# Kernel tuning notes

Hardware: AMD Instinct MI355X
Metric: run time of the kernel (lower is better)

Reference implementation:

```python
import jax, jax.numpy as jnp
import numpy as np

B, E, K = 2048, 16, 4
D_SF, D_OF, D_PPF, D_PVF = 512, 512, 256, 256
D = D_SF + D_OF + D_PPF + D_PVF  # 1536 = moe_input_size
H = 1024
N_OBJ, N_PRED = 36, 132
EPS = float(np.finfo(np.float64).eps)  # matches np.finfo(float).eps in combine
NOISE_EPS = 1e-2


def setup_inputs() -> dict:
    key = jax.random.key(0)
    ks = jax.random.split(key, 12)
    r = lambda i, shape, scale=1.0: (jax.random.normal(ks[i], shape, jnp.float32) * scale)
    return {
        "sf": r(0, (B, D_SF)),
        "of": r(1, (B, D_OF)),
        "ppf": r(2, (B, D_PPF)),
        "pvf": r(3, (B, D_PVF)),
        "w_gate": r(4, (D, E), 0.02),
        "w_noise": r(5, (D, E), 0.02),
        "W1": r(6, (E, D, H), 1.0 / np.sqrt(D)),
        "b1": jnp.zeros((E, H), jnp.float32),
        "W2": r(7, (E, H, H), 1.0 / np.sqrt(H)),
        "b2": jnp.zeros((E, H), jnp.float32),
        "Ws": r(8, (E, H, N_OBJ), 1.0 / np.sqrt(H)),
        "bs": jnp.zeros((E, N_OBJ), jnp.float32),
        "Wo": r(9, (E, H, N_OBJ), 1.0 / np.sqrt(H)),
        "bo": jnp.zeros((E, N_OBJ), jnp.float32),
        "Wp": r(10, (E, H, N_PRED), 1.0 / np.sqrt(H)),
        "bp": jnp.zeros((E, N_PRED), jnp.float32),
        "noise": r(11, (B, E)),
    }


def _noisy_top_k_gates(x, w_gate, w_noise, noise):
    """Shazeer noisy top-k gating -> sparse [B, E] gate matrix."""
    clean_logits = x @ w_gate                                   # [B, E]
    noise_stddev = jax.nn.softplus(x @ w_noise) + NOISE_EPS      # [B, E]
    logits = clean_logits + noise * noise_stddev
    top_vals, top_idx = jax.lax.top_k(logits, K)                 # [B, K]
    top_gates = jax.nn.softmax(top_vals, axis=-1)                # renormalized over top-k
    gates = jnp.zeros_like(logits)
    gates = gates.at[jnp.arange(x.shape[0])[:, None], top_idx].set(top_gates)
    return gates


def _combine(log_scores, gates):
    """SparseDispatcher.combine_expert_output, dense-equivalent.
    log_scores: [E, B, C] per-expert log-probs; gates: [B, E].
    output[b] = log(sum_e gates[b,e] * exp(log_scores[e,b])), eps where all-zero.
    gates==0 exactly zeroes the non-routed experts (same as sparse index_add).
    """
    w = gates.T[:, :, None]                                      # [E, B, 1]
    combined = jnp.sum(jnp.exp(log_scores) * w, axis=0)          # [B, C]
    combined = jnp.where(combined == 0, EPS, combined)
    return jnp.log(combined)


def reference(sf, of, ppf, pvf, w_gate, w_noise,
              W1, b1, W2, b2, Ws, bs, Wo, bo, Wp, bp, noise):
    x = jnp.concatenate([sf, of, ppf, pvf], axis=-1)             # [B, D]
    gates = _noisy_top_k_gates(x, w_gate, w_noise, noise)        # [B, E]

    # All-expert dense evaluation (grouped GEMM): 3-layer relu MLP trunk.
    h1 = jax.nn.relu(jnp.einsum('bd,edh->ebh', x, W1) + b1[:, None, :])   # [E, B, H]
    h2 = jax.nn.relu(jnp.einsum('ebh,ehg->ebg', h1, W2) + b2[:, None, :])  # [E, B, H]

    s_log = jax.nn.log_softmax(jnp.einsum('ebh,ehc->ebc', h2, Ws) + bs[:, None, :], axis=-1)
    o_log = jax.nn.log_softmax(jnp.einsum('ebh,ehc->ebc', h2, Wo) + bo[:, None, :], axis=-1)
    p_log = jax.nn.log_softmax(jnp.einsum('ebh,ehc->ebc', h2, Wp) + bp[:, None, :], axis=-1)

    s_out = _combine(s_log, gates)   # [B, N_OBJ]
    o_out = _combine(o_log, gates)   # [B, N_OBJ]
    p_out = _combine(p_log, gates)   # [B, N_PRED]
    return s_out, o_out, p_out
```

## Files before the change

kernel.cpp:

```cpp
#include <hip/hip_runtime.h>
#include <hip/hip_bf16.h>
#include <cstdint>

typedef __attribute__((ext_vector_type(8))) short short8;
typedef __attribute__((ext_vector_type(4))) float f32x4;

constexpr int B_ = 2048, E_ = 16, D_ = 1536, H_ = 1024;
constexpr int NHEAD = 256;
constexpr int TOTROWS = B_ * 4;
constexpr int MAXTILES = 80;
constexpr float EPS_ = 2.220446049250313e-16f;

__device__ __forceinline__ void gload_lds16(const void* g, void* l) {
  __builtin_amdgcn_global_load_lds((const __attribute__((address_space(1))) void*)g,
                                   (__attribute__((address_space(3))) void*)l,
                                   16, 0, 0);
}

__global__ __launch_bounds__(64) void zero_small(int* __restrict__ p, int n) {
  if ((int)threadIdx.x < n) p[threadIdx.x] = 0;
}

__global__ __launch_bounds__(256) void gate_logits(
    const float* __restrict__ sf, const float* __restrict__ of_,
    const float* __restrict__ ppf, const float* __restrict__ pvf,
    const float* __restrict__ wg, const float* __restrict__ wn,
    float* __restrict__ logits_all)
{
  __shared__ float xs[8][D_];
  const int b0 = blockIdx.x * 8;
  const int t = threadIdx.x;
  for (int i = t; i < 8 * (D_ / 4); i += 256) {
    const int row = i / (D_ / 4);
    const int c4 = i % (D_ / 4);
    const int b = b0 + row;
    const int d = c4 * 4;
    float4 v;
    if (d < 512)       v = ((const float4*)(sf  + (size_t)b * 512))[c4];
    else if (d < 1024) v = ((const float4*)(of_ + (size_t)b * 512))[c4 - 128];
    else if (d < 1280) v = ((const float4*)(ppf + (size_t)b * 256))[c4 - 256];
    else               v = ((const float4*)(pvf + (size_t)b * 256))[c4 - 320];
    *(float4*)&xs[row][d] = v;
  }
  __syncthreads();
  const int tok = t >> 5, out = t & 31;
  const int col = out & 15;
  const float* __restrict__ w = (out < 16) ? wg : wn;
  float a0 = 0.f, a1 = 0.f, a2 = 0.f, a3 = 0.f;
#pragma unroll 4
  for (int d = 0; d < D_; d += 4) {
    a0 += xs[tok][d + 0] * w[(d + 0) * 16 + col];
    a1 += xs[tok][d + 1] * w[(d + 1) * 16 + col];
    a2 += xs[tok][d + 2] * w[(d + 2) * 16 + col];
    a3 += xs[tok][d + 3] * w[(d + 3) * 16 + col];
  }
  logits_all[(size_t)(b0 + tok) * 32 + out] = (a0 + a1) + (a2 + a3);
}

__global__ __launch_bounds__(256) void topk_kernel(
    const float* __restrict__ logits_all, const float* __restrict__ noise,
    int* __restrict__ topidx, float* __restrict__ topw, int* __restrict__ counts)
{
  __shared__ int hist[E_];
  const int t = threadIdx.x;
  if (t < E_) hist[t] = 0;
  __syncthreads();
  const int b = blockIdx.x * 256 + t;
  if (b < B_) {
    float lg[16];
#pragma unroll
    for (int i = 0; i < 16; ++i) {
      const float clean = logits_all[(size_t)b * 32 + i];
      const float z = logits_all[(size_t)b * 32 + 16 + i];
      const float sp = (z > 0.f) ? (z + log1pf(expf(-z))) : log1pf(expf(z));
      lg[i] = clean + noise[b * 16 + i] * (sp + 1e-2f);
    }
    float tv[4]; int ti[4];
    unsigned used = 0;
#pragma unroll
    for (int k = 0; k < 4; ++k) {
      float best = -INFINITY; int bi = 0;
#pragma unroll
      for (int i = 0; i < 16; ++i)
        if (!((used >> i) & 1u) && lg[i] > best) { best = lg[i]; bi = i; }
      used |= 1u << bi; tv[k] = best; ti[k] = bi;
    }
    float s = 0.f, ex[4];
#pragma unroll
    for (int k = 0; k < 4; ++k) { ex[k] = expf(tv[k] - tv[0]); s += ex[k]; }
#pragma unroll
    for (int k = 0; k < 4; ++k) {
      topw[b * 4 + k] = ex[k] / s; topidx[b * 4 + k] = ti[k];
      atomicAdd(&hist[ti[k]], 1);
    }
  }
  __syncthreads();
  if (t < E_) atomicAdd(&counts[t], hist[t]);
}

__global__ __launch_bounds__(64) void schedule_kernel(
    const int* __restrict__ counts, int* __restrict__ offsets, int* __restrict__ ntiles,
    int* __restrict__ tile_e, int* __restrict__ tile_rb, int* __restrict__ tile_len)
{
  if (threadIdx.x != 0) return;
  int off = 0, nt = 0;
  for (int e = 0; e < E_; ++e) {
    offsets[e] = off;
    int c = counts[e];
    if (c < 0) c = 0;
    if (c > TOTROWS) c = TOTROWS;
    for (int m0 = 0; m0 < c && nt < MAXTILES; m0 += 128) {
      tile_e[nt] = e; tile_rb[nt] = off + m0;
      tile_len[nt] = (c - m0 < 128) ? (c - m0) : 128;
      ++nt;
    }
    off += c;
  }
  offsets[E_] = off;
  *ntiles = nt;
}

__global__ __launch_bounds__(256) void build_rows(
    const int* __restrict__ topidx, const int* __restrict__ offsets,
    int* __restrict__ cursor, int* __restrict__ rowtok, int* __restrict__ slot)
{
  const int b = blockIdx.x * 256 + threadIdx.x;
  if (b >= B_) return;
#pragma unroll
  for (int k = 0; k < 4; ++k) {
    const int e = topidx[b * 4 + k];
    const int p = atomicAdd(&cursor[e], 1);
    int row = offsets[e] + p;
    if (row < 0) row = 0;
    if (row >= TOTROWS) row = TOTROWS - 1;
    rowtok[row] = b;
    slot[b * 4 + k] = row;
  }
}

__global__ __launch_bounds__(256) void gather_x(
    const float* __restrict__ sf, const float* __restrict__ of_,
    const float* __restrict__ ppf, const float* __restrict__ pvf,
    const int* __restrict__ rowtok, __hip_bfloat16* __restrict__ xp)
{
  const int row = blockIdx.x;
  int b = rowtok[row];
  if (b < 0) b = 0;
  if (b >= B_) b = B_ - 1;
  for (int d = threadIdx.x; d < D_; d += 256) {
    float v;
    if (d < 512)       v = sf[b * 512 + d];
    else if (d < 1024) v = of_[b * 512 + (d - 512)];
    else if (d < 1280) v = ppf[b * 256 + (d - 1024)];
    else               v = pvf[b * 256 + (d - 1280)];
    xp[(size_t)row * D_ + d] = __float2bfloat16(v);
  }
}

__global__ __launch_bounds__(256) void transpose_bf16(
    const float* __restrict__ src, __hip_bfloat16* __restrict__ dst, int K, int N)
{
  __shared__ float tile[32][33];
  const int e = blockIdx.z;
  const int n0 = blockIdx.x * 32, k0 = blockIdx.y * 32;
  const int tx = threadIdx.x, ty = threadIdx.y;
  const float* s = src + (size_t)e * K * N;
  __hip_bfloat16* d = dst + (size_t)e * N * K;
#pragma unroll
  for (int r = 0; r < 4; ++r) {
    const int k = k0 + ty + r * 8;
    tile[ty + r * 8][tx] = s[(size_t)k * N + n0 + tx];
  }
  __syncthreads();
#pragma unroll
  for (int r = 0; r < 4; ++r) {
    const int n = n0 + ty + r * 8;
    d[(size_t)n * K + k0 + tx] = __float2bfloat16(tile[tx][ty + r * 8]);
  }
}

__global__ __launch_bounds__(256) void head_transpose(
    const float* __restrict__ Wsp, const float* __restrict__ Wop,
    const float* __restrict__ Wpp, __hip_bfloat16* __restrict__ dst)
{
  __shared__ float tile[32][33];
  const int e = blockIdx.z;
  const int k0 = blockIdx.x * 32;
  const int n0 = blockIdx.y * 32;
  const int tx = threadIdx.x, ty = threadIdx.y;
#pragma unroll
  for (int r = 0; r < 4; ++r) {
    const int k = k0 + ty + r * 8;
    const int n = n0 + tx;
    float v;
    if (n < 36)       v = Wsp[((size_t)e * H_ + k) * 36 + n];
    else if (n < 72)  v = Wop[((size_t)e * H_ + k) * 36 + (n - 36)];
    else if (n < 204) v = Wpp[((size_t)e * H_ + k) * 132 + (n - 72)];
    else              v = 0.f;
    tile[ty + r * 8][tx] = v;
  }
  __syncthreads();
#pragma unroll
  for (int r = 0; r < 4; ++r) {
    const int n = n0 + ty + r * 8;
    dst[((size_t)e * NHEAD + n) * H_ + k0 + tx] = __float2bfloat16(tile[tx][ty + r * 8]);
  }
}

__global__ __launch_bounds__(256) void pack_hbias(
    const float* __restrict__ bs, const float* __restrict__ bo,
    const float* __restrict__ bp, float* __restrict__ hb)
{
  const int e = blockIdx.x, t = threadIdx.x;
  float v = 0.f;
  if (t < 36)       v = bs[e * 36 + t];
  else if (t < 72)  v = bo[e * 36 + (t - 36)];
  else if (t < 204) v = bp[e * 132 + (t - 72)];
  hb[e * NHEAD + t] = v;
}

template <int EPI>
__global__ __launch_bounds__(256) void gemm_sp(
    const int* __restrict__ ntiles, const int* __restrict__ tile_e,
    const int* __restrict__ tile_rb, const int* __restrict__ tile_len,
    const __hip_bfloat16* __restrict__ Ap, int ldA,
    const __hip_bfloat16* __restrict__ Bm, size_t strideB,
    const float* __restrict__ bias,
    void* __restrict__ Cout, int ldC, int K)
{
  __shared__ __align__(16) __hip_bfloat16 lA[128 * 64];
  __shared__ __align__(16) __hip_bfloat16 lB[128 * 64];
  const int ti = blockIdx.x;
  int nt = *ntiles;
  if (nt > MAXTILES) nt = MAXTILES;
  if (ti >= nt) return;
  const int e = tile_e[ti] & 15, rb = tile_rb[ti], L = tile_len[ti];
  const int bn = blockIdx.y;
  const int t = threadIdx.x;
  const int w = t >> 6, lane = t & 63;
  const int wm = w >> 1, wn = w & 1;
  const __hip_bfloat16* Be = Bm + (size_t)e * strideB + (size_t)(bn * 128) * K;
  const int rsub = lane >> 3;
  const int csub = (lane & 7) * 8;

  int arows[4];
#pragma unroll
  for (int j = 0; j < 4; ++j) {
    int rloc = j * 32 + w * 8 + rsub;
    int r = rb + (rloc < L ? rloc : L - 1);
    if (r < 0) r = 0;
    if (r >= TOTROWS) r = TOTROWS - 1;
    arows[j] = r;
  }

  f32x4 acc[4][4];
#pragma unroll
  for (int m = 0; m < 4; ++m)
#pragma unroll
    for (int n = 0; n < 4; ++n) acc[m][n] = (f32x4){0.f, 0.f, 0.f, 0.f};

  const int KT = K >> 6;
  const int arow = wm * 64 + (lane & 15);
  const int brow = wn * 64 + (lane & 15);
  const int khalf = (lane >> 4) * 8;

  for (int kt = 0; kt < KT; ++kt) {
    const int k0 = kt << 6;
    __syncthreads();
#pragma unroll
    for (int j = 0; j < 4; ++j) {
      const int r = j * 32 + w * 8 + rsub;
      gload_lds16(Ap + (size_t)arows[j] * ldA + (k0 + csub), &lA[j * 2048 + w * 512]);
      gload_lds16(Be + (size_t)r * K + (k0 + csub), &lB[j * 2048 + w * 512]);
    }
    asm volatile("s_waitcnt vmcnt(0)" ::: "memory");
    __syncthreads();
#pragma unroll
    for (int kk = 0; kk < 2; ++kk) {
      short8 af[4], bfr[4];
#pragma unroll
      for (int m = 0; m < 4; ++m)
        af[m] = *(const short8*)&lA[(arow + m * 16) * 64 + kk * 32 + khalf];
#pragma unroll
      for (int n = 0; n < 4; ++n)
        bfr[n] = *(const short8*)&lB[(brow + n * 16) * 64 + kk * 32 + khalf];
#pragma unroll
      for (int m = 0; m < 4; ++m)
#pragma unroll
        for (int n = 0; n < 4; ++n)
          acc[m][n] = __builtin_amdgcn_mfma_f32_16x16x32_bf16(af[m], bfr[n], acc[m][n], 0, 0, 0);
    }
  }

  const int rbase = (lane >> 4) * 4, cbase = lane & 15;
#pragma unroll
  for (int n = 0; n < 4; ++n) {
    const int gcol = bn * 128 + wn * 64 + n * 16 + cbase;
    const float bv = bias[(size_t)e * ldC + gcol];
#pragma unroll
    for (int m = 0; m < 4; ++m) {
      const int rloc0 = wm * 64 + m * 16 + rbase;
#pragma unroll
      for (int j = 0; j < 4; ++j) {
        const int rloc = rloc0 + j;
        if (rloc < L && rb + rloc < TOTROWS) {
          float v = acc[m][n][j] + bv;
          const size_t idx = (size_t)(rb + rloc) * ldC + gcol;
          if (EPI == 0) {
            ((__hip_bfloat16*)Cout)[idx] = __float2bfloat16(v > 0.f ? v : 0.f);
          } else {
            ((float*)Cout)[idx] = v;
          }
        }
      }
    }
  }
}

__global__ __launch_bounds__(256) void combine_kernel(
    const float* __restrict__ logits, const int* __restrict__ slot,
    const float* __restrict__ topw, float* __restrict__ out)
{
  __shared__ float rows[4][204];
  __shared__ float lse[4][3];
  __shared__ float wk[4];
  const int b = blockIdx.x, t = threadIdx.x;
  if (t < 4) wk[t] = topw[b * 4 + t];
#pragma unroll
  for (int k = 0; k < 4; ++k) {
    int row = slot[b * 4 + k];
    if (row < 0) row = 0;
    if (row >= TOTROWS) row = TOTROWS - 1;
    if (t < 204) rows[k][t] = logits[(size_t)row * NHEAD + t];
  }
  __syncthreads();
  const int wv = t >> 6, lane = t & 63;
  const int segbase[3] = {0, 36, 72};
  const int segcnt[3] = {36, 36, 132};
  for (int s = 0; s < 3; ++s) {
    float mx = -INFINITY;
    for (int c = lane; c < segcnt[s]; c += 64) mx = fmaxf(mx, rows[wv][segbase[s] + c]);
    for (int o = 32; o > 0; o >>= 1) mx = fmaxf(mx, __shfl_xor(mx, o));
    float sum = 0.f;
    for (int c = lane; c < segcnt[s]; c += 64) sum += expf(rows[wv][segbase[s] + c] - mx);
    for (int o = 32; o > 0; o >>= 1) sum += __shfl_xor(sum, o);
    if (lane == 0) lse[wv][s] = mx + logf(sum);
  }
  __syncthreads();
  if (t < 204) {
    const int seg = t < 36 ? 0 : (t < 72 ? 1 : 2);
    float acc = 0.f;
    for (int k = 0; k < 4; ++k) acc += wk[k] * expf(rows[k][t] - lse[k][seg]);
    if (acc == 0.f) acc = EPS_;
    const float r = logf(acc);
    if (t < 36)      out[b * 36 + t] = r;
    else if (t < 72) out[73728 + b * 36 + (t - 36)] = r;
    else             out[147456 + b * 132 + (t - 72)] = r;
  }
}

extern "C" void kernel_launch(void* const* d_in, const int* in_sizes, int n_in,
                              void* d_out, int out_size, void* d_ws, size_t ws_size,
                              hipStream_t stream)
{
  (void)in_sizes; (void)n_in; (void)out_size; (void)ws_size;
  const float* sf      = (const float*)d_in[0];
  const float* of_     = (const float*)d_in[1];
  const float* ppf     = (const float*)d_in[2];
  const float* pvf     = (const float*)d_in[3];
  const float* w_gate  = (const float*)d_in[4];
  const float* w_noise = (const float*)d_in[5];
  const float* W1      = (const float*)d_in[6];
  const float* b1      = (const float*)d_in[7];
  const float* W2      = (const float*)d_in[8];
  const float* b2      = (const float*)d_in[9];
  const float* Ws      = (const float*)d_in[10];
  const float* bs      = (const float*)d_in[11];
  const float* Wo      = (const float*)d_in[12];
  const float* bo      = (const float*)d_in[13];
  const float* Wp      = (const float*)d_in[14];
  const float* bp      = (const float*)d_in[15];
  const float* noise   = (const float*)d_in[16];

  char* ws = (char*)d_ws;
  size_t off = 0;
  auto take = [&](size_t bytes) -> void* {
    void* p = ws + off; off += (bytes + 255) & ~(size_t)255; return p;
  };
  __hip_bfloat16* W1T = (__hip_bfloat16*)take((size_t)E_ * H_ * D_ * 2);
  __hip_bfloat16* W2T = (__hip_bfloat16*)take((size_t)E_ * H_ * H_ * 2);
  __hip_bfloat16* WhT = (__hip_bfloat16*)take((size_t)E_ * NHEAD * H_ * 2);
  float* hbias        = (float*)take((size_t)E_ * NHEAD * 4);
  __hip_bfloat16* xp  = (__hip_bfloat16*)take((size_t)TOTROWS * D_ * 2);
  __hip_bfloat16* h1p = (__hip_bfloat16*)take((size_t)TOTROWS * H_ * 2);
  __hip_bfloat16* h2p = (__hip_bfloat16*)take((size_t)TOTROWS * H_ * 2);
  float* logitsp      = (float*)take((size_t)TOTROWS * NHEAD * 4);
  float* logits_all   = (float*)take((size_t)B_ * 32 * 4);
  int* counts         = (int*)take(64 * 4);
  int* cursor         = (int*)take(64 * 4);
  int* offsets        = (int*)take(64 * 4);
  int* ntiles         = (int*)take(64 * 4);
  int* tile_e         = (int*)take(MAXTILES * 4);
  int* tile_rb        = (int*)take(MAXTILES * 4);
  int* tile_len       = (int*)take(MAXTILES * 4);
  int* topidx         = (int*)take((size_t)B_ * 4 * 4);
  float* topw         = (float*)take((size_t)B_ * 4 * 4);
  int* rowtok         = (int*)take((size_t)TOTROWS * 4);
  int* slot           = (int*)take((size_t)B_ * 4 * 4);

  zero_small<<<1, 64, 0, stream>>>(counts, E_);
  zero_small<<<1, 64, 0, stream>>>(cursor, E_);
  gate_logits<<<B_ / 8, 256, 0, stream>>>(sf, of_, ppf, pvf, w_gate, w_noise, logits_all);
  topk_kernel<<<B_ / 256, 256, 0, stream>>>(logits_all, noise, topidx, topw, counts);
  schedule_kernel<<<1, 64, 0, stream>>>(counts, offsets, ntiles, tile_e, tile_rb, tile_len);
  build_rows<<<(B_ + 255) / 256, 256, 0, stream>>>(topidx, offsets, cursor, rowtok, slot);
  gather_x<<<TOTROWS, 256, 0, stream>>>(sf, of_, ppf, pvf, rowtok, xp);

  transpose_bf16<<<dim3(H_ / 32, D_ / 32, E_), dim3(32, 8), 0, stream>>>(W1, W1T, D_, H_);
  transpose_bf16<<<dim3(H_ / 32, H_ / 32, E_), dim3(32, 8), 0, stream>>>(W2, W2T, H_, H_);
  head_transpose<<<dim3(H_ / 32, NHEAD / 32, E_), dim3(32, 8), 0, stream>>>(Ws, Wo, Wp, WhT);
  pack_hbias<<<E_, 256, 0, stream>>>(bs, bo, bp, hbias);

  gemm_sp<0><<<dim3(MAXTILES, H_ / 128), 256, 0, stream>>>(
      ntiles, tile_e, tile_rb, tile_len, xp, D_, W1T, (size_t)H_ * D_, b1, h1p, H_, D_);
  gemm_sp<0><<<dim3(MAXTILES, H_ / 128), 256, 0, stream>>>(
      ntiles, tile_e, tile_rb, tile_len, h1p, H_, W2T, (size_t)H_ * H_, b2, h2p, H_, H_);
  gemm_sp<1><<<dim3(MAXTILES, NHEAD / 128), 256, 0, stream>>>(
      ntiles, tile_e, tile_rb, tile_len, h2p, H_, WhT, (size_t)NHEAD * H_, hbias, logitsp, NHEAD, H_);

  combine_kernel<<<B_, 256, 0, stream>>>(logitsp, slot, topw, (float*)d_out);
}
```

Before: 567.4 us.

## Halve GEMM row tiles and fuse token gather into first expert GEMM

Expert GEMM tiles shrink from 128 to 64 rows (MAXTILES raised to 144). This gives more blocks, less padding waste on partially filled expert tiles, and better spread across CUs. The separate gather_x pass, which wrote a bf16 copy of x for every routed row, is replaced by a single per-token pack_x. The first GEMM now gathers A rows through rowtok. The two zeroing launches are merged into one 128-thread kernel covering both counts and cursor. The trade-off is that each weight tile is now loaded from memory for twice as many row tiles, raising B-operand traffic.

```diff
diff --git a/kernel.cpp b/kernel.cpp
--- a/kernel.cpp
+++ b/kernel.cpp
@@ -8,7 +8,7 @@
 constexpr int B_ = 2048, E_ = 16, D_ = 1536, H_ = 1024;
 constexpr int NHEAD = 256;
 constexpr int TOTROWS = B_ * 4;
-constexpr int MAXTILES = 80;
+constexpr int MAXTILES = 144;
 constexpr float EPS_ = 2.220446049250313e-16f;
 
 __device__ __forceinline__ void gload_lds16(const void* g, void* l) {
@@ -17,8 +17,24 @@
                                    16, 0, 0);
 }
 
-__global__ __launch_bounds__(64) void zero_small(int* __restrict__ p, int n) {
-  if ((int)threadIdx.x < n) p[threadIdx.x] = 0;
+__global__ __launch_bounds__(128) void zero128(int* __restrict__ p) {
+  p[threadIdx.x] = 0;
+}
+
+__global__ __launch_bounds__(256) void pack_x(
+    const float* __restrict__ sf, const float* __restrict__ of_,
+    const float* __restrict__ ppf, const float* __restrict__ pvf,
+    __hip_bfloat16* __restrict__ xb)
+{
+  const int b = blockIdx.x;
+  for (int d = threadIdx.x; d < D_; d += 256) {
+    float v;
+    if (d < 512)       v = sf[b * 512 + d];
+    else if (d < 1024) v = of_[b * 512 + (d - 512)];
+    else if (d < 1280) v = ppf[b * 256 + (d - 1024)];
+    else               v = pvf[b * 256 + (d - 1280)];
+    xb[(size_t)b * D_ + d] = __float2bfloat16(v);
+  }
 }
 
 __global__ __launch_bounds__(256) void gate_logits(
@@ -109,9 +125,9 @@
     int c = counts[e];
     if (c < 0) c = 0;
     if (c > TOTROWS) c = TOTROWS;
-    for (int m0 = 0; m0 < c && nt < MAXTILES; m0 += 128) {
+    for (int m0 = 0; m0 < c && nt < MAXTILES; m0 += 64) {
       tile_e[nt] = e; tile_rb[nt] = off + m0;
-      tile_len[nt] = (c - m0 < 128) ? (c - m0) : 128;
+      tile_len[nt] = (c - m0 < 64) ? (c - m0) : 64;
       ++nt;
     }
     off += c;
@@ -135,25 +151,6 @@
     if (row >= TOTROWS) row = TOTROWS - 1;
     rowtok[row] = b;
     slot[b * 4 + k] = row;
-  }
-}
-
-__global__ __launch_bounds__(256) void gather_x(
-    const float* __restrict__ sf, const float* __restrict__ of_,
-    const float* __restrict__ ppf, const float* __restrict__ pvf,
-    const int* __restrict__ rowtok, __hip_bfloat16* __restrict__ xp)
-{
-  const int row = blockIdx.x;
-  int b = rowtok[row];
-  if (b < 0) b = 0;
-  if (b >= B_) b = B_ - 1;
-  for (int d = threadIdx.x; d < D_; d += 256) {
-    float v;
-    if (d < 512)       v = sf[b * 512 + d];
-    else if (d < 1024) v = of_[b * 512 + (d - 512)];
-    else if (d < 1280) v = ppf[b * 256 + (d - 1024)];
-    else               v = pvf[b * 256 + (d - 1280)];
-    xp[(size_t)row * D_ + d] = __float2bfloat16(v);
   }
 }
 
@@ -219,16 +216,17 @@
   hb[e * NHEAD + t] = v;
 }
 
-template <int EPI>
+template <int EPI, int GATHER>
 __global__ __launch_bounds__(256) void gemm_sp(
     const int* __restrict__ ntiles, const int* __restrict__ tile_e,
     const int* __restrict__ tile_rb, const int* __restrict__ tile_len,
+    const int* __restrict__ rowtok,
     const __hip_bfloat16* __restrict__ Ap, int ldA,
     const __hip_bfloat16* __restrict__ Bm, size_t strideB,
     const float* __restrict__ bias,
     void* __restrict__ Cout, int ldC, int K)
 {
-  __shared__ __align__(16) __hip_bfloat16 lA[128 * 64];
+  __shared__ __align__(16) __hip_bfloat16 lA[64 * 64];
   __shared__ __align__(16) __hip_bfloat16 lB[128 * 64];
   const int ti = blockIdx.x;
   int nt = *ntiles;
@@ -240,27 +238,32 @@
   const int w = t >> 6, lane = t & 63;
   const int wm = w >> 1, wn = w & 1;
   const __hip_bfloat16* Be = Bm + (size_t)e * strideB + (size_t)(bn * 128) * K;
-  const int rsub = lane >> 3;
-  const int csub = (lane & 7) * 8;
-
-  int arows[4];
-#pragma unroll
-  for (int j = 0; j < 4; ++j) {
-    int rloc = j * 32 + w * 8 + rsub;
+  const int srow = t >> 3;
+  const int scol = (t & 7) * 8;
+
+  int asrc[2];
+#pragma unroll
+  for (int j = 0; j < 2; ++j) {
+    const int rloc = j * 32 + srow;
     int r = rb + (rloc < L ? rloc : L - 1);
     if (r < 0) r = 0;
     if (r >= TOTROWS) r = TOTROWS - 1;
-    arows[j] = r;
-  }
-
-  f32x4 acc[4][4];
-#pragma unroll
-  for (int m = 0; m < 4; ++m)
+    if (GATHER) {
+      r = rowtok[r];
+      if (r < 0) r = 0;
+      if (r >= B_) r = B_ - 1;
+    }
+    asrc[j] = r;
+  }
+
+  f32x4 acc[2][4];
+#pragma unroll
+  for (int m = 0; m < 2; ++m)
 #pragma unroll
     for (int n = 0; n < 4; ++n) acc[m][n] = (f32x4){0.f, 0.f, 0.f, 0.f};
 
   const int KT = K >> 6;
-  const int arow = wm * 64 + (lane & 15);
+  const int arow = wm * 32 + (lane & 15);
   const int brow = wn * 64 + (lane & 15);
   const int khalf = (lane >> 4) * 8;
 
@@ -268,24 +271,24 @@
     const int k0 = kt << 6;
     __syncthreads();
 #pragma unroll
-    for (int j = 0; j < 4; ++j) {
-      const int r = j * 32 + w * 8 + rsub;
-      gload_lds16(Ap + (size_t)arows[j] * ldA + (k0 + csub), &lA[j * 2048 + w * 512]);
-      gload_lds16(Be + (size_t)r * K + (k0 + csub), &lB[j * 2048 + w * 512]);
-    }
+    for (int j = 0; j < 2; ++j)
+      gload_lds16(Ap + (size_t)asrc[j] * ldA + (k0 + scol), lA + j * 2048 + t * 8);
+#pragma unroll
+    for (int j = 0; j < 4; ++j)
+      gload_lds16(Be + (size_t)(j * 32 + srow) * K + (k0 + scol), lB + j * 2048 + t * 8);
     asm volatile("s_waitcnt vmcnt(0)" ::: "memory");
     __syncthreads();
 #pragma unroll
     for (int kk = 0; kk < 2; ++kk) {
-      short8 af[4], bfr[4];
-#pragma unroll
-      for (int m = 0; m < 4; ++m)
+      short8 af[2], bfr[4];
+#pragma unroll
+      for (int m = 0; m < 2; ++m)
         af[m] = *(const short8*)&lA[(arow + m * 16) * 64 + kk * 32 + khalf];
 #pragma unroll
       for (int n = 0; n < 4; ++n)
         bfr[n] = *(const short8*)&lB[(brow + n * 16) * 64 + kk * 32 + khalf];
 #pragma unroll
-      for (int m = 0; m < 4; ++m)
+      for (int m = 0; m < 2; ++m)
 #pragma unroll
         for (int n = 0; n < 4; ++n)
           acc[m][n] = __builtin_amdgcn_mfma_f32_16x16x32_bf16(af[m], bfr[n], acc[m][n], 0, 0, 0);
@@ -298,8 +301,8 @@
     const int gcol = bn * 128 + wn * 64 + n * 16 + cbase;
     const float bv = bias[(size_t)e * ldC + gcol];
 #pragma unroll
-    for (int m = 0; m < 4; ++m) {
-      const int rloc0 = wm * 64 + m * 16 + rbase;
+    for (int m = 0; m < 2; ++m) {
+      const int rloc0 = wm * 32 + m * 16 + rbase;
 #pragma unroll
       for (int j = 0; j < 4; ++j) {
         const int rloc = rloc0 + j;
@@ -391,7 +394,7 @@
   __hip_bfloat16* W2T = (__hip_bfloat16*)take((size_t)E_ * H_ * H_ * 2);
   __hip_bfloat16* WhT = (__hip_bfloat16*)take((size_t)E_ * NHEAD * H_ * 2);
   float* hbias        = (float*)take((size_t)E_ * NHEAD * 4);
-  __hip_bfloat16* xp  = (__hip_bfloat16*)take((size_t)TOTROWS * D_ * 2);
+  __hip_bfloat16* xb  = (__hip_bfloat16*)take((size_t)B_ * D_ * 2);
   __hip_bfloat16* h1p = (__hip_bfloat16*)take((size_t)TOTROWS * H_ * 2);
   __hip_bfloat16* h2p = (__hip_bfloat16*)take((size_t)TOTROWS * H_ * 2);
   float* logitsp      = (float*)take((size_t)TOTROWS * NHEAD * 4);
@@ -408,25 +411,27 @@
   int* rowtok         = (int*)take((size_t)TOTROWS * 4);
   int* slot           = (int*)take((size_t)B_ * 4 * 4);
 
-  zero_small<<<1, 64, 0, stream>>>(counts, E_);
-  zero_small<<<1, 64, 0, stream>>>(cursor, E_);
+  zero128<<<1, 128, 0, stream>>>(counts);
   gate_logits<<<B_ / 8, 256, 0, stream>>>(sf, of_, ppf, pvf, w_gate, w_noise, logits_all);
   topk_kernel<<<B_ / 256, 256, 0, stream>>>(logits_all, noise, topidx, topw, counts);
   schedule_kernel<<<1, 64, 0, stream>>>(counts, offsets, ntiles, tile_e, tile_rb, tile_len);
   build_rows<<<(B_ + 255) / 256, 256, 0, stream>>>(topidx, offsets, cursor, rowtok, slot);
-  gather_x<<<TOTROWS, 256, 0, stream>>>(sf, of_, ppf, pvf, rowtok, xp);
+  pack_x<<<B_, 256, 0, stream>>>(sf, of_, ppf, pvf, xb);
 
   transpose_bf16<<<dim3(H_ / 32, D_ / 32, E_), dim3(32, 8), 0, stream>>>(W1, W1T, D_, H_);
   transpose_bf16<<<dim3(H_ / 32, H_ / 32, E_), dim3(32, 8), 0, stream>>>(W2, W2T, H_, H_);
   head_transpose<<<dim3(H_ / 32, NHEAD / 32, E_), dim3(32, 8), 0, stream>>>(Ws, Wo, Wp, WhT);
   pack_hbias<<<E_, 256, 0, stream>>>(bs, bo, bp, hbias);
 
-  gemm_sp<0><<<dim3(MAXTILES, H_ / 128), 256, 0, stream>>>(
-      ntiles, tile_e, tile_rb, tile_len, xp, D_, W1T, (size_t)H_ * D_, b1, h1p, H_, D_);
-  gemm_sp<0><<<dim3(MAXTILES, H_ / 128), 256, 0, stream>>>(
-      ntiles, tile_e, tile_rb, tile_len, h1p, H_, W2T, (size_t)H_ * H_, b2, h2p, H_, H_);
-  gemm_sp<1><<<dim3(MAXTILES, NHEAD / 128), 256, 0, stream>>>(
-      ntiles, tile_e, tile_rb, tile_len, h2p, H_, WhT, (size_t)NHEAD * H_, hbias, logitsp, NHEAD, H_);
+  gemm_sp<0, 1><<<dim3(MAXTILES, H_ / 128), 256, 0, stream>>>(
+      ntiles, tile_e, tile_rb, tile_len, rowtok, xb, D_, W1T, (size_t)H_ * D_, b1,
+      h1p, H_, D_);
+  gemm_sp<0, 0><<<dim3(MAXTILES, H_ / 128), 256, 0, stream>>>(
+      ntiles, tile_e, tile_rb, tile_len, rowtok, h1p, H_, W2T, (size_t)H_ * H_, b2,
+      h2p, H_, H_);
+  gemm_sp<1, 0><<<dim3(MAXTILES, NHEAD / 128), 256, 0, stream>>>(
+      ntiles, tile_e, tile_rb, tile_len, rowtok, h2p, H_, WhT, (size_t)NHEAD * H_, hbias,
+      logitsp, NHEAD, H_);
 
   combine_kernel<<<B_, 256, 0, stream>>>(logitsp, slot, topw, (float*)d_out);
 }
```

Measured after the change: 529.1 us. 6.7% less time.
